# Kernel optimization log

Measured on AMD Instinct MI355X. Metric: run time of the kernel, lower is better.

Reference implementation:

```python
import jax, jax.numpy as jnp
import numpy as np

N_NODES = 2_000_000
N_EDGES = 16_777_216
N_REL = 4


def setup_inputs() -> dict:
    key = jax.random.key(0)
    ks = jax.random.split(key, 13)
    inp = {
        "author_x": jax.random.normal(ks[0], (N_NODES, 4), jnp.float32),
        "paper_x": jax.random.normal(ks[1], (N_NODES, 4), jnp.float32),
        "src_index": jax.random.randint(ks[2], (N_EDGES,), 0, N_NODES, jnp.int64 if jax.config.jax_enable_x64 else jnp.int32).astype(jnp.int32),
        "dst_index": jax.random.randint(ks[3], (N_EDGES,), 0, N_NODES).astype(jnp.int32),
        "edge_type_index": jax.random.randint(ks[4], (N_EDGES,), 0, N_REL).astype(jnp.int32),
        "edge_src_is_paper": jax.random.randint(ks[5], (N_REL,), 0, 2).astype(jnp.int32),
        "edge_dst_is_paper": jax.random.randint(ks[6], (N_REL,), 0, 2).astype(jnp.int32),
        "Wa": jax.random.normal(ks[7], (4, 4), jnp.float32) * 0.5,
        "ba": jax.random.normal(ks[8], (4,), jnp.float32) * 0.1,
        "Wp": jax.random.normal(ks[9], (4, 4), jnp.float32) * 0.5,
        "bp": jax.random.normal(ks[10], (4,), jnp.float32) * 0.1,
        "Ws": jax.random.normal(ks[11], (8,), jnp.float32) * 0.5,
        "bs": jax.random.normal(ks[12], (1,), jnp.float32) * 0.1,
    }
    return inp


def reference(author_x, paper_x, src_index, dst_index, edge_type_index,
              edge_src_is_paper, edge_dst_is_paper, Wa, ba, Wp, bp, Ws, bs):
    # Encode node tables (tiny GEMMs): [N,4] @ [4,4]^T + [4]
    author_h = author_x @ Wa.T + ba
    paper_h = paper_x @ Wp.T + bp
    # Per-edge relation-type dispatch: 1 = paper table, 0 = author table
    src_p = edge_src_is_paper[edge_type_index].astype(bool)  # [E]
    dst_p = edge_dst_is_paper[edge_type_index].astype(bool)  # [E]
    src_repr = jnp.where(src_p[:, None], paper_h[src_index], author_h[src_index])  # [E,4]
    dst_repr = jnp.where(dst_p[:, None], paper_h[dst_index], author_h[dst_index])  # [E,4]
    # scorer: Linear(8,1) on concat, squeeze last dim -> [E]
    logits = jnp.concatenate([src_repr, dst_repr], axis=-1) @ Ws + bs[0]
    return logits
```

## Files before the change

### kernel.cpp

```cpp
#include <hip/hip_runtime.h>

typedef int         iv4 __attribute__((ext_vector_type(4)));
typedef float       fv4 __attribute__((ext_vector_type(4)));
typedef _Float16    hv4 __attribute__((ext_vector_type(4)));
typedef signed char cv4 __attribute__((ext_vector_type(4)));

struct Fold {
    float va_s[4], va_d[4], vp_s[4], vp_d[4];
    float ca_s, ca_d, cp_s, cp_d;
};

__device__ inline Fold make_fold(const float* __restrict__ Wa, const float* __restrict__ ba,
                                 const float* __restrict__ Wp, const float* __restrict__ bp,
                                 const float* __restrict__ Ws) {
    Fold f;
    float w0 = Ws[0], w1 = Ws[1], w2 = Ws[2], w3 = Ws[3];
    float w4 = Ws[4], w5 = Ws[5], w6 = Ws[6], w7 = Ws[7];
#pragma unroll
    for (int j = 0; j < 4; ++j) {
        f.va_s[j] = w0*Wa[j] + w1*Wa[4+j] + w2*Wa[8+j] + w3*Wa[12+j];
        f.va_d[j] = w4*Wa[j] + w5*Wa[4+j] + w6*Wa[8+j] + w7*Wa[12+j];
        f.vp_s[j] = w0*Wp[j] + w1*Wp[4+j] + w2*Wp[8+j] + w3*Wp[12+j];
        f.vp_d[j] = w4*Wp[j] + w5*Wp[4+j] + w6*Wp[8+j] + w7*Wp[12+j];
    }
    f.ca_s = w0*ba[0] + w1*ba[1] + w2*ba[2] + w3*ba[3];
    f.ca_d = w4*ba[0] + w5*ba[1] + w6*ba[2] + w7*ba[3];
    f.cp_s = w0*bp[0] + w1*bp[1] + w2*bp[2] + w3*bp[3];
    f.cp_d = w4*bp[0] + w5*bp[1] + w6*bp[2] + w7*bp[3];
    return f;
}

__device__ inline void node_scores(const Fold& f, fv4 a, fv4 p,
                                   float& as, float& ps, float& ad, float& pd) {
    as = a.x*f.va_s[0] + a.y*f.va_s[1] + a.z*f.va_s[2] + a.w*f.va_s[3] + f.ca_s;
    ad = a.x*f.va_d[0] + a.y*f.va_d[1] + a.z*f.va_d[2] + a.w*f.va_d[3] + f.ca_d;
    ps = p.x*f.vp_s[0] + p.y*f.vp_s[1] + p.z*f.vp_s[2] + p.w*f.vp_s[3] + f.cp_s;
    pd = p.x*f.vp_d[0] + p.y*f.vp_d[1] + p.z*f.vp_d[2] + p.w*f.vp_d[3] + f.cp_d;
}

__global__ __launch_bounds__(256) void node_pass1(
    const fv4* __restrict__ ax, const fv4* __restrict__ px,
    const float* __restrict__ Wa, const float* __restrict__ ba,
    const float* __restrict__ Wp, const float* __restrict__ bp,
    const float* __restrict__ Ws,
    hv4* __restrict__ sc, unsigned* __restrict__ maxes, int n)
{
    Fold f = make_fold(Wa, ba, Wp, bp, Ws);
    float ms = 0.f, md = 0.f;
    int stride = gridDim.x * blockDim.x;
    for (int i = blockIdx.x * blockDim.x + threadIdx.x; i < n; i += stride) {
        fv4 a = __builtin_nontemporal_load(ax + i);
        fv4 p = __builtin_nontemporal_load(px + i);
        float as, ps, ad, pd;
        node_scores(f, a, p, as, ps, ad, pd);
        hv4 h;
        h.x = (_Float16)as; h.y = (_Float16)ps; h.z = (_Float16)ad; h.w = (_Float16)pd;
        __builtin_nontemporal_store(h, sc + i);
        ms = fmaxf(ms, fmaxf(fabsf(as), fabsf(ps)));
        md = fmaxf(md, fmaxf(fabsf(ad), fabsf(pd)));
    }
#pragma unroll
    for (int off = 32; off >= 1; off >>= 1) {
        ms = fmaxf(ms, __shfl_down(ms, off));
        md = fmaxf(md, __shfl_down(md, off));
    }
    __shared__ float lms[4], lmd[4];
    int wave = threadIdx.x >> 6, lane = threadIdx.x & 63;
    if (lane == 0) { lms[wave] = ms; lmd[wave] = md; }
    __syncthreads();
    if (threadIdx.x == 0) {
        float bms = fmaxf(fmaxf(lms[0], lms[1]), fmaxf(lms[2], lms[3]));
        float bmd = fmaxf(fmaxf(lmd[0], lmd[1]), fmaxf(lmd[2], lmd[3]));
        atomicMax(&maxes[0], __float_as_uint(bms));
        atomicMax(&maxes[1], __float_as_uint(bmd));
    }
}

__global__ __launch_bounds__(256) void node_pass2(
    const hv4* __restrict__ sc, const unsigned* __restrict__ maxes,
    signed char* __restrict__ ts, signed char* __restrict__ td, int n)
{
    int i = blockIdx.x * blockDim.x + threadIdx.x;
    if (i >= n) return;
    float inv_s = 127.f / fmaxf(__uint_as_float(maxes[0]), 1e-20f);
    float inv_d = 127.f / fmaxf(__uint_as_float(maxes[1]), 1e-20f);
    hv4 h = __builtin_nontemporal_load(sc + i);
    int qas = min(127, max(-127, __float2int_rn((float)h.x * inv_s)));
    int qps = min(127, max(-127, __float2int_rn((float)h.y * inv_s)));
    int qad = min(127, max(-127, __float2int_rn((float)h.z * inv_d)));
    int qpd = min(127, max(-127, __float2int_rn((float)h.w * inv_d)));
    cv4 dummy;
    (void)dummy;
    ((short*)ts)[i] = (short)(((qps & 0xff) << 8) | (qas & 0xff));
    ((short*)td)[i] = (short)(((qpd & 0xff) << 8) | (qad & 0xff));
}

__global__ __launch_bounds__(256) void edge_src_pass(
    const iv4* __restrict__ src, const iv4* __restrict__ et,
    const int* __restrict__ esp,
    const signed char* __restrict__ ts, cv4* __restrict__ qsrc, int n4)
{
    int i = blockIdx.x * blockDim.x + threadIdx.x;
    if (i >= n4) return;
    unsigned smask = (unsigned)((esp[0]&1) | ((esp[1]&1)<<1) | ((esp[2]&1)<<2) | ((esp[3]&1)<<3));
    iv4 s = __builtin_nontemporal_load(src + i);
    iv4 t = __builtin_nontemporal_load(et  + i);
    cv4 q;
    q.x = ts[2*s.x + (int)((smask >> t.x) & 1u)];
    q.y = ts[2*s.y + (int)((smask >> t.y) & 1u)];
    q.z = ts[2*s.z + (int)((smask >> t.z) & 1u)];
    q.w = ts[2*s.w + (int)((smask >> t.w) & 1u)];
    __builtin_nontemporal_store(q, qsrc + i);
}

__global__ __launch_bounds__(256) void edge_dst_pass(
    const iv4* __restrict__ dst, const iv4* __restrict__ et,
    const int* __restrict__ edp, const float* __restrict__ bs,
    const unsigned* __restrict__ maxes,
    const signed char* __restrict__ td, const cv4* __restrict__ qsrc,
    fv4* __restrict__ out, int n4)
{
    int i = blockIdx.x * blockDim.x + threadIdx.x;
    if (i >= n4) return;
    unsigned dmask = (unsigned)((edp[0]&1) | ((edp[1]&1)<<1) | ((edp[2]&1)<<2) | ((edp[3]&1)<<3));
    float b = bs[0];
    float scale_s = __uint_as_float(maxes[0]) * (1.f / 127.f);
    float scale_d = __uint_as_float(maxes[1]) * (1.f / 127.f);

    iv4 d = __builtin_nontemporal_load(dst + i);
    iv4 t = __builtin_nontemporal_load(et  + i);
    cv4 qs = __builtin_nontemporal_load(qsrc + i);
    signed char q0 = td[2*d.x + (int)((dmask >> t.x) & 1u)];
    signed char q1 = td[2*d.y + (int)((dmask >> t.y) & 1u)];
    signed char q2 = td[2*d.z + (int)((dmask >> t.z) & 1u)];
    signed char q3 = td[2*d.w + (int)((dmask >> t.w) & 1u)];

    fv4 o;
    o.x = (float)qs.x * scale_s + (float)q0 * scale_d + b;
    o.y = (float)qs.y * scale_s + (float)q1 * scale_d + b;
    o.z = (float)qs.z * scale_s + (float)q2 * scale_d + b;
    o.w = (float)qs.w * scale_s + (float)q3 * scale_d + b;
    __builtin_nontemporal_store(o, out + i);
}

__global__ __launch_bounds__(256) void fused_kernel(
    const fv4* __restrict__ ax, const fv4* __restrict__ px,
    const int* __restrict__ src, const int* __restrict__ dst, const int* __restrict__ et,
    const int* __restrict__ esp, const int* __restrict__ edp,
    const float* __restrict__ Wa, const float* __restrict__ ba,
    const float* __restrict__ Wp, const float* __restrict__ bp,
    const float* __restrict__ Ws, const float* __restrict__ bs,
    float* __restrict__ out, int n)
{
    int e = blockIdx.x * blockDim.x + threadIdx.x;
    if (e >= n) return;
    Fold f = make_fold(Wa, ba, Wp, bp, Ws);
    int t = et[e];
    int sp = esp[t] & 1, dp = edp[t] & 1;
    fv4 sv = sp ? px[src[e]] : ax[src[e]];
    fv4 dv = dp ? px[dst[e]] : ax[dst[e]];
    float ssc = sp ? (sv.x*f.vp_s[0] + sv.y*f.vp_s[1] + sv.z*f.vp_s[2] + sv.w*f.vp_s[3] + f.cp_s)
                   : (sv.x*f.va_s[0] + sv.y*f.va_s[1] + sv.z*f.va_s[2] + sv.w*f.va_s[3] + f.ca_s);
    float dsc = dp ? (dv.x*f.vp_d[0] + dv.y*f.vp_d[1] + dv.z*f.vp_d[2] + dv.w*f.vp_d[3] + f.cp_d)
                   : (dv.x*f.va_d[0] + dv.y*f.va_d[1] + dv.z*f.va_d[2] + dv.w*f.va_d[3] + f.ca_d);
    out[e] = ssc + dsc + bs[0];
}

extern "C" void kernel_launch(void* const* d_in, const int* in_sizes, int n_in,
                              void* d_out, int out_size, void* d_ws, size_t ws_size,
                              hipStream_t stream) {
    const float* ax  = (const float*)d_in[0];
    const float* px  = (const float*)d_in[1];
    const int*   src = (const int*)d_in[2];
    const int*   dst = (const int*)d_in[3];
    const int*   et  = (const int*)d_in[4];
    const int*   esp = (const int*)d_in[5];
    const int*   edp = (const int*)d_in[6];
    const float* Wa  = (const float*)d_in[7];
    const float* ba  = (const float*)d_in[8];
    const float* Wp  = (const float*)d_in[9];
    const float* bp  = (const float*)d_in[10];
    const float* Ws  = (const float*)d_in[11];
    const float* bs  = (const float*)d_in[12];
    float* out = (float*)d_out;

    const int n_nodes = in_sizes[0] / 4;
    const int n_edges = in_sizes[2];

    size_t union_sz = (size_t)n_edges > (size_t)n_nodes * 8 ? (size_t)n_edges : (size_t)n_nodes * 8;
    union_sz = (union_sz + 255) & ~(size_t)255;
    const size_t off_u  = 256;
    const size_t off_ts = off_u + union_sz;
    const size_t off_td = off_ts + (size_t)n_nodes * 2;
    const size_t need   = off_td + (size_t)n_nodes * 2;

    if (ws_size >= need && (n_edges & 3) == 0) {
        unsigned* maxes = (unsigned*)d_ws;
        hv4* sc   = (hv4*)((char*)d_ws + off_u);
        cv4* qsrc = (cv4*)((char*)d_ws + off_u);
        signed char* ts = (signed char*)((char*)d_ws + off_ts);
        signed char* td = (signed char*)((char*)d_ws + off_td);

        (void)hipMemsetAsync(maxes, 0, 2 * sizeof(unsigned), stream);
        node_pass1<<<512, 256, 0, stream>>>(
            (const fv4*)ax, (const fv4*)px, Wa, ba, Wp, bp, Ws, sc, maxes, n_nodes);
        node_pass2<<<(n_nodes + 255) / 256, 256, 0, stream>>>(
            sc, maxes, ts, td, n_nodes);

        const int n4 = n_edges / 4;
        const int nb = (n4 + 255) / 256;
        edge_src_pass<<<nb, 256, 0, stream>>>(
            (const iv4*)src, (const iv4*)et, esp, ts, qsrc, n4);
        edge_dst_pass<<<nb, 256, 0, stream>>>(
            (const iv4*)dst, (const iv4*)et, edp, bs, maxes,
            td, (const cv4*)qsrc, (fv4*)out, n4);
    } else {
        fused_kernel<<<(n_edges + 255) / 256, 256, 0, stream>>>(
            (const fv4*)ax, (const fv4*)px, src, dst, et, esp, edp,
            Wa, ba, Wp, bp, Ws, bs, out, n_edges);
    }
}
```

Before: 433.8 us.

## Fuse src and dst edge passes into one kernel processing eight edges per thread

Merges the separate source-gather and destination-gather edge kernels into a single kernel. This removes the intermediate quantized-source buffer write and read, a second read of the edge-type array, and one launch. Each thread now handles eight edges with two vector loads per input stream for more memory-level parallelism. The node reduction kernel grid is also enlarged. Both int8 node tables must now stay cache-resident together during the fused gather.

```diff
diff --git a/kernel.cpp b/kernel.cpp
--- a/kernel.cpp
+++ b/kernel.cpp
@@ -89,58 +89,65 @@
     int qps = min(127, max(-127, __float2int_rn((float)h.y * inv_s)));
     int qad = min(127, max(-127, __float2int_rn((float)h.z * inv_d)));
     int qpd = min(127, max(-127, __float2int_rn((float)h.w * inv_d)));
-    cv4 dummy;
-    (void)dummy;
     ((short*)ts)[i] = (short)(((qps & 0xff) << 8) | (qas & 0xff));
     ((short*)td)[i] = (short)(((qpd & 0xff) << 8) | (qad & 0xff));
 }
 
-__global__ __launch_bounds__(256) void edge_src_pass(
-    const iv4* __restrict__ src, const iv4* __restrict__ et,
-    const int* __restrict__ esp,
-    const signed char* __restrict__ ts, cv4* __restrict__ qsrc, int n4)
+__global__ __launch_bounds__(256) void edge_fused(
+    const iv4* __restrict__ src4, const iv4* __restrict__ dst4, const iv4* __restrict__ et4,
+    const int* __restrict__ esp, const int* __restrict__ edp,
+    const float* __restrict__ bs, const unsigned* __restrict__ maxes,
+    const signed char* __restrict__ ts, const signed char* __restrict__ td,
+    fv4* __restrict__ out4, int n8)
 {
     int i = blockIdx.x * blockDim.x + threadIdx.x;
-    if (i >= n4) return;
+    if (i >= n8) return;
     unsigned smask = (unsigned)((esp[0]&1) | ((esp[1]&1)<<1) | ((esp[2]&1)<<2) | ((esp[3]&1)<<3));
-    iv4 s = __builtin_nontemporal_load(src + i);
-    iv4 t = __builtin_nontemporal_load(et  + i);
-    cv4 q;
-    q.x = ts[2*s.x + (int)((smask >> t.x) & 1u)];
-    q.y = ts[2*s.y + (int)((smask >> t.y) & 1u)];
-    q.z = ts[2*s.z + (int)((smask >> t.z) & 1u)];
-    q.w = ts[2*s.w + (int)((smask >> t.w) & 1u)];
-    __builtin_nontemporal_store(q, qsrc + i);
-}
-
-__global__ __launch_bounds__(256) void edge_dst_pass(
-    const iv4* __restrict__ dst, const iv4* __restrict__ et,
-    const int* __restrict__ edp, const float* __restrict__ bs,
-    const unsigned* __restrict__ maxes,
-    const signed char* __restrict__ td, const cv4* __restrict__ qsrc,
-    fv4* __restrict__ out, int n4)
-{
-    int i = blockIdx.x * blockDim.x + threadIdx.x;
-    if (i >= n4) return;
     unsigned dmask = (unsigned)((edp[0]&1) | ((edp[1]&1)<<1) | ((edp[2]&1)<<2) | ((edp[3]&1)<<3));
     float b = bs[0];
     float scale_s = __uint_as_float(maxes[0]) * (1.f / 127.f);
     float scale_d = __uint_as_float(maxes[1]) * (1.f / 127.f);
 
-    iv4 d = __builtin_nontemporal_load(dst + i);
-    iv4 t = __builtin_nontemporal_load(et  + i);
-    cv4 qs = __builtin_nontemporal_load(qsrc + i);
-    signed char q0 = td[2*d.x + (int)((dmask >> t.x) & 1u)];
-    signed char q1 = td[2*d.y + (int)((dmask >> t.y) & 1u)];
-    signed char q2 = td[2*d.z + (int)((dmask >> t.z) & 1u)];
-    signed char q3 = td[2*d.w + (int)((dmask >> t.w) & 1u)];
-
-    fv4 o;
-    o.x = (float)qs.x * scale_s + (float)q0 * scale_d + b;
-    o.y = (float)qs.y * scale_s + (float)q1 * scale_d + b;
-    o.z = (float)qs.z * scale_s + (float)q2 * scale_d + b;
-    o.w = (float)qs.w * scale_s + (float)q3 * scale_d + b;
-    __builtin_nontemporal_store(o, out + i);
+    iv4 s0 = __builtin_nontemporal_load(src4 + 2*i);
+    iv4 s1 = __builtin_nontemporal_load(src4 + 2*i + 1);
+    iv4 d0 = __builtin_nontemporal_load(dst4 + 2*i);
+    iv4 d1 = __builtin_nontemporal_load(dst4 + 2*i + 1);
+    iv4 t0 = __builtin_nontemporal_load(et4 + 2*i);
+    iv4 t1 = __builtin_nontemporal_load(et4 + 2*i + 1);
+
+    int as0 = 2*s0.x + (int)((smask >> t0.x) & 1u);
+    int as1 = 2*s0.y + (int)((smask >> t0.y) & 1u);
+    int as2 = 2*s0.z + (int)((smask >> t0.z) & 1u);
+    int as3 = 2*s0.w + (int)((smask >> t0.w) & 1u);
+    int as4 = 2*s1.x + (int)((smask >> t1.x) & 1u);
+    int as5 = 2*s1.y + (int)((smask >> t1.y) & 1u);
+    int as6 = 2*s1.z + (int)((smask >> t1.z) & 1u);
+    int as7 = 2*s1.w + (int)((smask >> t1.w) & 1u);
+    int ad0 = 2*d0.x + (int)((dmask >> t0.x) & 1u);
+    int ad1 = 2*d0.y + (int)((dmask >> t0.y) & 1u);
+    int ad2 = 2*d0.z + (int)((dmask >> t0.z) & 1u);
+    int ad3 = 2*d0.w + (int)((dmask >> t0.w) & 1u);
+    int ad4 = 2*d1.x + (int)((dmask >> t1.x) & 1u);
+    int ad5 = 2*d1.y + (int)((dmask >> t1.y) & 1u);
+    int ad6 = 2*d1.z + (int)((dmask >> t1.z) & 1u);
+    int ad7 = 2*d1.w + (int)((dmask >> t1.w) & 1u);
+
+    signed char qs0 = ts[as0], qs1 = ts[as1], qs2 = ts[as2], qs3 = ts[as3];
+    signed char qs4 = ts[as4], qs5 = ts[as5], qs6 = ts[as6], qs7 = ts[as7];
+    signed char qd0 = td[ad0], qd1 = td[ad1], qd2 = td[ad2], qd3 = td[ad3];
+    signed char qd4 = td[ad4], qd5 = td[ad5], qd6 = td[ad6], qd7 = td[ad7];
+
+    fv4 o0, o1;
+    o0.x = (float)qs0 * scale_s + (float)qd0 * scale_d + b;
+    o0.y = (float)qs1 * scale_s + (float)qd1 * scale_d + b;
+    o0.z = (float)qs2 * scale_s + (float)qd2 * scale_d + b;
+    o0.w = (float)qs3 * scale_s + (float)qd3 * scale_d + b;
+    o1.x = (float)qs4 * scale_s + (float)qd4 * scale_d + b;
+    o1.y = (float)qs5 * scale_s + (float)qd5 * scale_d + b;
+    o1.z = (float)qs6 * scale_s + (float)qd6 * scale_d + b;
+    o1.w = (float)qs7 * scale_s + (float)qd7 * scale_d + b;
+    __builtin_nontemporal_store(o0, out4 + 2*i);
+    __builtin_nontemporal_store(o1, out4 + 2*i + 1);
 }
 
 __global__ __launch_bounds__(256) void fused_kernel(
@@ -187,33 +194,28 @@
     const int n_nodes = in_sizes[0] / 4;
     const int n_edges = in_sizes[2];
 
-    size_t union_sz = (size_t)n_edges > (size_t)n_nodes * 8 ? (size_t)n_edges : (size_t)n_nodes * 8;
-    union_sz = (union_sz + 255) & ~(size_t)255;
-    const size_t off_u  = 256;
-    const size_t off_ts = off_u + union_sz;
+    size_t sc_sz = ((size_t)n_nodes * 8 + 255) & ~(size_t)255;
+    const size_t off_sc = 256;
+    const size_t off_ts = off_sc + sc_sz;
     const size_t off_td = off_ts + (size_t)n_nodes * 2;
     const size_t need   = off_td + (size_t)n_nodes * 2;
 
-    if (ws_size >= need && (n_edges & 3) == 0) {
+    if (ws_size >= need && (n_edges & 7) == 0) {
         unsigned* maxes = (unsigned*)d_ws;
-        hv4* sc   = (hv4*)((char*)d_ws + off_u);
-        cv4* qsrc = (cv4*)((char*)d_ws + off_u);
+        hv4* sc   = (hv4*)((char*)d_ws + off_sc);
         signed char* ts = (signed char*)((char*)d_ws + off_ts);
         signed char* td = (signed char*)((char*)d_ws + off_td);
 
         (void)hipMemsetAsync(maxes, 0, 2 * sizeof(unsigned), stream);
-        node_pass1<<<512, 256, 0, stream>>>(
+        node_pass1<<<2048, 256, 0, stream>>>(
             (const fv4*)ax, (const fv4*)px, Wa, ba, Wp, bp, Ws, sc, maxes, n_nodes);
         node_pass2<<<(n_nodes + 255) / 256, 256, 0, stream>>>(
             sc, maxes, ts, td, n_nodes);
 
-        const int n4 = n_edges / 4;
-        const int nb = (n4 + 255) / 256;
-        edge_src_pass<<<nb, 256, 0, stream>>>(
-            (const iv4*)src, (const iv4*)et, esp, ts, qsrc, n4);
-        edge_dst_pass<<<nb, 256, 0, stream>>>(
-            (const iv4*)dst, (const iv4*)et, edp, bs, maxes,
-            td, (const cv4*)qsrc, (fv4*)out, n4);
+        const int n8 = n_edges / 8;
+        edge_fused<<<(n8 + 255) / 256, 256, 0, stream>>>(
+            (const iv4*)src, (const iv4*)dst, (const iv4*)et, esp, edp,
+            bs, maxes, ts, td, (fv4*)out, n8);
     } else {
         fused_kernel<<<(n_edges + 255) / 256, 256, 0, stream>>>(
             (const fv4*)ax, (const fv4*)px, src, dst, et, esp, edp,
```

New measurement: 565.8 us. 1.3x slower.
